# Kernel optimization log

Measured on AMD Instinct MI355X. Metric: run time of the kernel, lower is better.

Reference implementation:

```python
import jax, jax.numpy as jnp
import numpy as np

BATCH = 32768
INPUT_DIM = 256
N_NEURONS = 128
MAX_DEGREE = 7  # D; features per input dim = D+1 = 8


def _cheb_features(x, degree):
    """Chebyshev T_0..T_degree of x [B, In] -> [B, In, degree+1] via recurrence.

    Matches torch.special.chebyshev_polynomial_t(x, n=d) for d = 0..degree.
    """
    T = [jnp.ones_like(x), x]
    for _ in range(2, degree + 1):
        T.append(2.0 * x * T[-1] - T[-2])
    return jnp.stack(T[: degree + 1], axis=-1)


def setup_inputs() -> dict:
    key = jax.random.key(0)
    k1, k2 = jax.random.split(key)
    # inputs in [0,1) keep Chebyshev values bounded, as in a normalized pipeline
    x = jax.random.uniform(k1, (BATCH, INPUT_DIM), dtype=jnp.float32)
    # per-neuron coefficient vectors over the dim-major [In*(D+1)] feature layout
    coeffs = jax.random.normal(k2, (N_NEURONS, INPUT_DIM * (MAX_DEGREE + 1)), dtype=jnp.float32) * 0.02
    return {"x": x, "coeffs": coeffs}


def reference(x, coeffs):
    B, In = x.shape
    D = coeffs.shape[1] // In - 1
    # [B, In, D+1] -> dim-major flatten matches torch.cat over per-dim stacks
    X = _cheb_features(x, D).reshape(B, In * (D + 1))
    # per-neuron dot products, then sum over neurons (KANLayer stack().sum(0))
    per_neuron = jnp.einsum("bf,nf->bn", X, coeffs)  # [B, n_neurons]
    return per_neuron.sum(axis=1, keepdims=True)  # [B, 1]
```

## Files before the change

### kernel.cpp

```cpp
#include <hip/hip_runtime.h>

#define BATCH     32768
#define IN_DIM    256
#define N_NEURONS 128
#define DEG1      8
#define FEAT      (IN_DIM * DEG1)
#define ROWS_PER_WAVE 8

__global__ __launch_bounds__(256) void reduce_coeffs(const float* __restrict__ coeffs,
                                                     float* __restrict__ csum) {
    __shared__ float part[4][64];
    const int t = threadIdx.x;
    const int f_local = t & 63;
    const int ng = t >> 6;
    const int f = blockIdx.x * 64 + f_local;
    float s = 0.f;
    const float* p = coeffs + (size_t)(ng * 32) * FEAT + f;
#pragma unroll
    for (int n = 0; n < 32; ++n) s += p[(size_t)n * FEAT];
    part[ng][f_local] = s;
    __syncthreads();
    if (ng == 0) {
        csum[f] = part[0][f_local] + part[1][f_local] + part[2][f_local] + part[3][f_local];
    }
}

__global__ __launch_bounds__(256) void kan_fwd(const float* __restrict__ x,
                                               const float* __restrict__ csum,
                                               float* __restrict__ out) {
    const int lane = threadIdx.x & 63;
    const int wave = threadIdx.x >> 6;
    const int row0 = (blockIdx.x * 4 + wave) * ROWS_PER_WAVE;

    float c[4][8];
    const float4* c4 = (const float4*)csum + (size_t)lane * 8;
#pragma unroll
    for (int j = 0; j < 4; ++j) {
        float4 a = c4[j * 2];
        float4 b = c4[j * 2 + 1];
        c[j][0] = a.x; c[j][1] = a.y; c[j][2] = a.z; c[j][3] = a.w;
        c[j][4] = b.x; c[j][5] = b.y; c[j][6] = b.z; c[j][7] = b.w;
    }

    float acc[ROWS_PER_WAVE];
    const float4* xr = (const float4*)x + (size_t)row0 * (IN_DIM / 4) + lane;

#pragma unroll
    for (int r = 0; r < ROWS_PER_WAVE; ++r) {
        float4 xv = xr[(size_t)r * (IN_DIM / 4)];
        float xs[4] = {xv.x, xv.y, xv.z, xv.w};
        float a = 0.f;
#pragma unroll
        for (int j = 0; j < 4; ++j) {
            const float xx = xs[j];
            const float two_x = xx + xx;
            a = fmaf(c[j][1], xx, a + c[j][0]);
            float tp = 1.f, tc = xx;
#pragma unroll
            for (int d = 2; d < 8; ++d) {
                float tn = fmaf(two_x, tc, -tp);
                a = fmaf(c[j][d], tn, a);
                tp = tc; tc = tn;
            }
        }
        acc[r] = a;
    }

#pragma unroll
    for (int r = 0; r < ROWS_PER_WAVE; ++r) {
        float a = acc[r];
#pragma unroll
        for (int off = 32; off > 0; off >>= 1) a += __shfl_down(a, off, 64);
        if (lane == 0) out[row0 + r] = a;
    }
}

extern "C" void kernel_launch(void* const* d_in, const int* in_sizes, int n_in,
                              void* d_out, int out_size, void* d_ws, size_t ws_size,
                              hipStream_t stream) {
    const float* x      = (const float*)d_in[0];
    const float* coeffs = (const float*)d_in[1];
    float* out  = (float*)d_out;
    float* csum = (float*)d_ws;

    reduce_coeffs<<<FEAT / 64, 256, 0, stream>>>(coeffs, csum);
    kan_fwd<<<BATCH / (4 * ROWS_PER_WAVE), 256, 0, stream>>>(x, csum, out);
}
```

Before: 78.65 us.

## Vectorize coefficient reduction, double rows per wave, store outputs as float4

The coefficient-sum kernel now reads float4 columns across 64 blocks and combines them with a shared-memory tree reduction. Before, it used 32 blocks of scalar strided loads. The forward kernel processes 16 rows per wave instead of 8, which halves the grid and spreads the per-thread coefficient register loads over more rows. Output rows are written as float4 by lane 0. The main risks are higher register pressure, lower occupancy, and the extra syncs in the reduction tree.

Result: no change. 77.69 us (-1.2%).

```diff
diff --git a/kernel.cpp b/kernel.cpp
--- a/kernel.cpp
+++ b/kernel.cpp
@@ -5,24 +5,39 @@
 #define N_NEURONS 128
 #define DEG1      8
 #define FEAT      (IN_DIM * DEG1)
-#define ROWS_PER_WAVE 8
+#define F4        (FEAT / 4)
+#define XR4       (IN_DIM / 4)
+#define RPW       16
 
 __global__ __launch_bounds__(256) void reduce_coeffs(const float* __restrict__ coeffs,
                                                      float* __restrict__ csum) {
-    __shared__ float part[4][64];
+    __shared__ float4 part[256];
     const int t = threadIdx.x;
-    const int f_local = t & 63;
-    const int ng = t >> 6;
-    const int f = blockIdx.x * 64 + f_local;
-    float s = 0.f;
-    const float* p = coeffs + (size_t)(ng * 32) * FEAT + f;
+    const int c = t & 7;
+    const int g = t >> 3;
+    const int col4 = blockIdx.x * 8 + c;
+
+    const float4* p = (const float4*)coeffs + (size_t)(g * 4) * F4 + col4;
+    float4 s = make_float4(0.f, 0.f, 0.f, 0.f);
 #pragma unroll
-    for (int n = 0; n < 32; ++n) s += p[(size_t)n * FEAT];
-    part[ng][f_local] = s;
+    for (int n = 0; n < 4; ++n) {
+        float4 v = p[(size_t)n * F4];
+        s.x += v.x; s.y += v.y; s.z += v.z; s.w += v.w;
+    }
+    part[t] = s;
     __syncthreads();
-    if (ng == 0) {
-        csum[f] = part[0][f_local] + part[1][f_local] + part[2][f_local] + part[3][f_local];
+
+#pragma unroll
+    for (int stride = 128; stride >= 8; stride >>= 1) {
+        if (t < stride) {
+            float4 o = part[t + stride];
+            float4 m = part[t];
+            m.x += o.x; m.y += o.y; m.z += o.z; m.w += o.w;
+            part[t] = m;
+        }
+        __syncthreads();
     }
+    if (t < 8) ((float4*)csum)[blockIdx.x * 8 + t] = part[t];
 }
 
 __global__ __launch_bounds__(256) void kan_fwd(const float* __restrict__ x,
@@ -30,7 +45,7 @@
                                                float* __restrict__ out) {
     const int lane = threadIdx.x & 63;
     const int wave = threadIdx.x >> 6;
-    const int row0 = (blockIdx.x * 4 + wave) * ROWS_PER_WAVE;
+    const int row0 = (blockIdx.x * 4 + wave) * RPW;
 
     float c[4][8];
     const float4* c4 = (const float4*)csum + (size_t)lane * 8;
@@ -42,12 +57,12 @@
         c[j][4] = b.x; c[j][5] = b.y; c[j][6] = b.z; c[j][7] = b.w;
     }
 
-    float acc[ROWS_PER_WAVE];
-    const float4* xr = (const float4*)x + (size_t)row0 * (IN_DIM / 4) + lane;
+    float acc[RPW];
+    const float4* xr = (const float4*)x + (size_t)row0 * XR4 + lane;
 
 #pragma unroll
-    for (int r = 0; r < ROWS_PER_WAVE; ++r) {
-        float4 xv = xr[(size_t)r * (IN_DIM / 4)];
+    for (int r = 0; r < RPW; ++r) {
+        float4 xv = xr[(size_t)r * XR4];
         float xs[4] = {xv.x, xv.y, xv.z, xv.w};
         float a = 0.f;
 #pragma unroll
@@ -67,11 +82,18 @@
     }
 
 #pragma unroll
-    for (int r = 0; r < ROWS_PER_WAVE; ++r) {
-        float a = acc[r];
+    for (int rq = 0; rq < RPW / 4; ++rq) {
+        float s[4];
 #pragma unroll
-        for (int off = 32; off > 0; off >>= 1) a += __shfl_down(a, off, 64);
-        if (lane == 0) out[row0 + r] = a;
+        for (int k = 0; k < 4; ++k) {
+            float a = acc[rq * 4 + k];
+#pragma unroll
+            for (int off = 32; off > 0; off >>= 1) a += __shfl_down(a, off, 64);
+            s[k] = a;
+        }
+        if (lane == 0) {
+            ((float4*)out)[row0 / 4 + rq] = make_float4(s[0], s[1], s[2], s[3]);
+        }
     }
 }
 
@@ -83,6 +105,6 @@
     float* out  = (float*)d_out;
     float* csum = (float*)d_ws;
 
-    reduce_coeffs<<<FEAT / 64, 256, 0, stream>>>(coeffs, csum);
-    kan_fwd<<<BATCH / (4 * ROWS_PER_WAVE), 256, 0, stream>>>(x, csum, out);
+    reduce_coeffs<<<64, 256, 0, stream>>>(coeffs, csum);
+    kan_fwd<<<BATCH / (4 * RPW), 256, 0, stream>>>(x, csum, out);
 }
```
